# Optimization experiments

Measured on AMD Instinct MI355X. Metric: run time of the kernel, lower is better.

The kernel has to match this reference:

```python
import jax, jax.numpy as jnp
import numpy as np
from jax import lax

B, T = 2, 2048
HID = 2048
H, K, KC = 16, 128, 4
D = H * K  # projection dim
EPS = 1e-5
SCALE = K ** -0.5


def causal_conv_silu(x, w, b):
    # x: [B,T,D], depthwise causal conv, w: [D,KC], b: [D]
    xp = jnp.pad(jnp.swapaxes(x, 1, 2), ((0, 0), (0, 0), (KC - 1, 0)))  # [B,D,T+KC-1]
    y = lax.conv_general_dilated(xp, w[:, None, :], (1,), 'VALID', feature_group_count=D)
    return jax.nn.silu(jnp.swapaxes(y, 1, 2) + b)


def l2norm(x):
    return x * lax.rsqrt(jnp.sum(x * x, -1, keepdims=True) + 1e-6)


def kda_scan(q, k, v, g, beta):
    # gated delta-rule linear recurrence (KDA), per-key-dim log decay g
    # q,k,v,g: [B,T,H,K]; beta: [B,T,H]
    qT, kT, vT, gT, bT = (jnp.moveaxis(a, 1, 0) for a in (q, k, v, g, beta))
    S0 = jnp.zeros((q.shape[0], H, K, K), q.dtype)  # state [B,H,K,V]

    def step(S, inp):
        qt, kt, vt, gt, bt = inp
        S = S * jnp.exp(gt)[..., None]                                   # decay along K
        vd = (vt - jnp.einsum('bhkv,bhk->bhv', S, kt)) * bt[..., None]   # delta-rule error * beta
        S = S + kt[..., None] * vd[:, :, None, :]                        # rank-1 update
        return S, jnp.einsum('bhkv,bhk->bhv', S, qt)

    _, o = lax.scan(step, S0, (qT, kT, vT, gT, bT))
    return jnp.moveaxis(o, 0, 1)  # [B,T,H,K]


def _forward(x, Wq, Wk, Wv, conv_q_w, conv_q_b, conv_k_w, conv_k_b, conv_v_w, conv_v_b,
             Wfa, Wfb, A_log, dt_bias, Wb, Wga, Wgb, o_norm_w, Wo):
    b, t = x.shape[:2]
    q = causal_conv_silu(x @ Wq, conv_q_w, conv_q_b).reshape(b, t, H, K)
    k = causal_conv_silu(x @ Wk, conv_k_w, conv_k_b).reshape(b, t, H, K)
    v = causal_conv_silu(x @ Wv, conv_v_w, conv_v_b).reshape(b, t, H, K)
    # fine-grained decay gate: g = -exp(A_log[h]) * softplus(f_b(f_a(x)) + dt_bias)
    g = jax.nn.softplus((x @ Wfa) @ Wfb + dt_bias).reshape(b, t, H, K)
    g = -jnp.exp(A_log)[None, None, :, None] * g
    beta = jax.nn.sigmoid(x @ Wb)  # [B,T,H]
    q = l2norm(q) * SCALE
    k = l2norm(k)
    o = kda_scan(q, k, v, g, beta)  # [B,T,H,K]
    # gated head-wise RMSNorm
    gate = ((x @ Wga) @ Wgb).reshape(b, t, H, K)
    var = jnp.mean(o * o, -1, keepdims=True)
    o = o * lax.rsqrt(var + EPS) * o_norm_w * jax.nn.sigmoid(gate)
    return o.reshape(b, t, D) @ Wo


def setup_inputs() -> dict:
    key = jax.random.key(0)
    ks = jax.random.split(key, 16)
    s = 0.02
    f32 = jnp.float32
    return {
        'x': jax.random.normal(ks[0], (B, T, HID), f32),
        'Wq': jax.random.normal(ks[1], (HID, D), f32) * s,
        'Wk': jax.random.normal(ks[2], (HID, D), f32) * s,
        'Wv': jax.random.normal(ks[3], (HID, D), f32) * s,
        'conv_q_w': jax.random.normal(ks[4], (D, KC), f32) * 0.2,
        'conv_q_b': jnp.zeros((D,), f32),
        'conv_k_w': jax.random.normal(ks[5], (D, KC), f32) * 0.2,
        'conv_k_b': jnp.zeros((D,), f32),
        'conv_v_w': jax.random.normal(ks[6], (D, KC), f32) * 0.2,
        'conv_v_b': jnp.zeros((D,), f32),
        'Wfa': jax.random.normal(ks[7], (HID, K), f32) * s,
        'Wfb': jax.random.normal(ks[8], (K, D), f32) * s,
        'A_log': jnp.log(jax.random.uniform(ks[9], (H,), f32, 1.0, 16.0)),
        'dt_bias': jnp.zeros((D,), f32),
        'Wb': jax.random.normal(ks[10], (HID, H), f32) * s,
        'Wga': jax.random.normal(ks[11], (HID, K), f32) * s,
        'Wgb': jax.random.normal(ks[12], (K, D), f32) * s,
        'o_norm_w': jnp.ones((K,), f32),
        'Wo': jax.random.normal(ks[13], (D, HID), f32) * s,
    }


def reference(x, Wq, Wk, Wv, conv_q_w, conv_q_b, conv_k_w, conv_k_b, conv_v_w, conv_v_b,
              Wfa, Wfb, A_log, dt_bias, Wb, Wga, Wgb, o_norm_w, Wo):
    return _forward(x, Wq, Wk, Wv, conv_q_w, conv_q_b, conv_k_w, conv_k_b, conv_v_w, conv_v_b,
                    Wfa, Wfb, A_log, dt_bias, Wb, Wga, Wgb, o_norm_w, Wo)
```

## Files before the change

kernel.cpp:

```cpp
#include <hip/hip_runtime.h>
#include <cstddef>

#define Bsz 2
#define Tt  2048
#define HIDc 2048
#define Hh  16
#define Kc  128
#define Dc  2048
#define BT  (Bsz*Tt)
#define TS  8

typedef __attribute__((ext_vector_type(8))) __bf16 bf16x8;
typedef __attribute__((ext_vector_type(4))) __bf16 bf16x4;
typedef __attribute__((ext_vector_type(4))) float f32x4;

__device__ __forceinline__ float epilogue(float vacc, int c, int mode,
                                          const float* __restrict__ alog,
                                          const float* __restrict__ dtb) {
    if (mode == 1) {
        float z  = vacc + dtb[c];
        float sp = fmaxf(z, 0.f) + log1pf(expf(-fabsf(z)));
        return expf(-expf(alog[c >> 7]) * sp);
    } else if (mode == 2) {
        return 1.f / (1.f + expf(-vacc));
    }
    return vacc;
}

__global__ __launch_bounds__(256) void gemm_bf16_mfma(
    const __bf16* __restrict__ A, const __bf16* __restrict__ Bw,
    float* __restrict__ C, int M, int N, int K)
{
    __shared__ __bf16 As[128 * 64];
    __shared__ __bf16 Bs[128 * 64];
    const int tid = threadIdx.x;
    const int lane = tid & 63;
    const int wave = tid >> 6;
    const int wr = wave >> 1, wc = wave & 1;
    const int l15 = lane & 15, g = lane >> 4;
    const int row0 = blockIdx.y * 128, col0 = blockIdx.x * 128;

    f32x4 acc[4][4];
#pragma unroll
    for (int m = 0; m < 4; m++)
#pragma unroll
        for (int n = 0; n < 4; n++)
            acc[m][n] = (f32x4){0.f, 0.f, 0.f, 0.f};

    for (int k0 = 0; k0 < K; k0 += 64) {
        __syncthreads();
#pragma unroll
        for (int i = 0; i < 4; i++) {
            const int c = i * 256 + tid;
            const int row = c >> 3, kc = c & 7;
            const int scol = k0 + 8 * (kc ^ (row & 7));
            __builtin_amdgcn_global_load_lds(
                (const __attribute__((address_space(1))) void*)(A + (size_t)(row0 + row) * K + scol),
                (__attribute__((address_space(3))) void*)(As + (size_t)(i * 256 + (tid & ~63)) * 8),
                16, 0, 0);
        }
#pragma unroll
        for (int i = 0; i < 4; i++) {
            const int c = i * 256 + tid;
            const int row = c >> 3, kc = c & 7;
            const int scol = k0 + 8 * (kc ^ (row & 7));
            __builtin_amdgcn_global_load_lds(
                (const __attribute__((address_space(1))) void*)(Bw + (size_t)(col0 + row) * K + scol),
                (__attribute__((address_space(3))) void*)(Bs + (size_t)(i * 256 + (tid & ~63)) * 8),
                16, 0, 0);
        }
        __syncthreads();
#pragma unroll
        for (int ks = 0; ks < 2; ks++) {
            bf16x8 af[4], bfr[4];
#pragma unroll
            for (int m = 0; m < 4; m++) {
                const int row = wr * 64 + m * 16 + l15;
                const int kc = ks * 4 + g;
                af[m] = *(const bf16x8*)(As + row * 64 + 8 * (kc ^ (row & 7)));
            }
#pragma unroll
            for (int n = 0; n < 4; n++) {
                const int col = wc * 64 + n * 16 + l15;
                const int kc = ks * 4 + g;
                bfr[n] = *(const bf16x8*)(Bs + col * 64 + 8 * (kc ^ (col & 7)));
            }
#pragma unroll
            for (int m = 0; m < 4; m++)
#pragma unroll
                for (int n = 0; n < 4; n++)
                    acc[m][n] = __builtin_amdgcn_mfma_f32_16x16x32_bf16(
                        af[m], bfr[n], acc[m][n], 0, 0, 0);
        }
    }
#pragma unroll
    for (int m = 0; m < 4; m++) {
        const int rbase = row0 + wr * 64 + m * 16 + g * 4;
#pragma unroll
        for (int n = 0; n < 4; n++) {
            const int col = col0 + wc * 64 + n * 16 + l15;
#pragma unroll
            for (int r = 0; r < 4; r++)
                C[(size_t)(rbase + r) * N + col] = acc[m][n][r];
        }
    }
}

__global__ __launch_bounds__(256) void cvt_bf16(
    const float* __restrict__ in, __bf16* __restrict__ o)
{
    const int i = blockIdx.x * 256 + threadIdx.x;
    float4 v = *(const float4*)(in + (size_t)4 * i);
    bf16x4 r;
    r[0] = (__bf16)v.x; r[1] = (__bf16)v.y; r[2] = (__bf16)v.z; r[3] = (__bf16)v.w;
    *(bf16x4*)(o + (size_t)4 * i) = r;
}

__global__ __launch_bounds__(256) void transpose_to_bf16(
    const float* __restrict__ W, __bf16* __restrict__ WT, int Kd, int N)
{
    __shared__ float tile[32][33];
    const int n0 = blockIdx.x * 32, k0 = blockIdx.y * 32;
    const int tx = threadIdx.x & 31, ty = threadIdx.x >> 5;
#pragma unroll
    for (int i = 0; i < 4; i++)
        tile[ty + 8 * i][tx] = W[(size_t)(k0 + ty + 8 * i) * N + n0 + tx];
    __syncthreads();
#pragma unroll
    for (int i = 0; i < 4; i++)
        WT[(size_t)(n0 + ty + 8 * i) * Kd + k0 + tx] = (__bf16)tile[tx][ty + 8 * i];
}

__global__ __launch_bounds__(256) void gemm_f32(
    const float* __restrict__ A, const float* __restrict__ B, float* __restrict__ C,
    int M, int N, int Kd, int mode,
    const float* __restrict__ alog, const float* __restrict__ dtb)
{
    __shared__ float As[8][128];
    __shared__ float Bs[8][128];
    const int tid = threadIdx.x;
    const int tx = tid & 15, ty = tid >> 4;
    const int rbase = blockIdx.y * 128, cbase = blockIdx.x * 128;
    const int z = blockIdx.z, Znum = gridDim.z;
    const int kchunk = Kd / Znum;
    const int kbeg = z * kchunk, kend = kbeg + kchunk;

    float acc[8][8];
#pragma unroll
    for (int i = 0; i < 8; i++)
#pragma unroll
        for (int j = 0; j < 8; j++) acc[i][j] = 0.f;

    const int arow = tid >> 1, ak = (tid & 1) << 2;
    const int bk = tid >> 5, bn = (tid & 31) << 2;

    for (int k0 = kbeg; k0 < kend; k0 += 8) {
        float4 av = *(const float4*)(A + (size_t)(rbase + arow) * Kd + (k0 + ak));
        float4 bv = make_float4(0.f, 0.f, 0.f, 0.f);
        if (cbase + bn < N)
            bv = *(const float4*)(B + (size_t)(k0 + bk) * N + (cbase + bn));
        __syncthreads();
        As[ak + 0][arow] = av.x;
        As[ak + 1][arow] = av.y;
        As[ak + 2][arow] = av.z;
        As[ak + 3][arow] = av.w;
        *(float4*)(&Bs[bk][bn]) = bv;
        __syncthreads();
#pragma unroll
        for (int kk = 0; kk < 8; ++kk) {
            float a[8], bb[8];
            *(float4*)(&a[0]) = *(const float4*)(&As[kk][ty << 2]);
            *(float4*)(&a[4]) = *(const float4*)(&As[kk][64 + (ty << 2)]);
            *(float4*)(&bb[0]) = *(const float4*)(&Bs[kk][tx << 2]);
            *(float4*)(&bb[4]) = *(const float4*)(&Bs[kk][64 + (tx << 2)]);
#pragma unroll
            for (int i = 0; i < 8; i++)
#pragma unroll
                for (int j = 0; j < 8; j++)
                    acc[i][j] = fmaf(a[i], bb[j], acc[i][j]);
        }
    }

    if (Znum > 1) {
        float* P = C + (size_t)z * M * N;
#pragma unroll
        for (int ih = 0; ih < 2; ih++)
#pragma unroll
            for (int i = 0; i < 4; i++) {
                int r = rbase + ih * 64 + (ty << 2) + i;
#pragma unroll
                for (int jh = 0; jh < 2; jh++) {
                    int c0 = cbase + jh * 64 + (tx << 2);
                    if (c0 < N) {
                        float4 vv;
                        vv.x = acc[ih * 4 + i][jh * 4 + 0];
                        vv.y = acc[ih * 4 + i][jh * 4 + 1];
                        vv.z = acc[ih * 4 + i][jh * 4 + 2];
                        vv.w = acc[ih * 4 + i][jh * 4 + 3];
                        *(float4*)(P + (size_t)r * N + c0) = vv;
                    }
                }
            }
    } else {
#pragma unroll
        for (int ih = 0; ih < 2; ih++)
#pragma unroll
            for (int i = 0; i < 4; i++) {
                int r = rbase + ih * 64 + (ty << 2) + i;
#pragma unroll
                for (int jh = 0; jh < 2; jh++) {
                    int c0 = cbase + jh * 64 + (tx << 2);
                    if (c0 < N) {
                        float4 vv;
                        vv.x = epilogue(acc[ih * 4 + i][jh * 4 + 0], c0 + 0, mode, alog, dtb);
                        vv.y = epilogue(acc[ih * 4 + i][jh * 4 + 1], c0 + 1, mode, alog, dtb);
                        vv.z = epilogue(acc[ih * 4 + i][jh * 4 + 2], c0 + 2, mode, alog, dtb);
                        vv.w = epilogue(acc[ih * 4 + i][jh * 4 + 3], c0 + 3, mode, alog, dtb);
                        *(float4*)(C + (size_t)r * N + c0) = vv;
                    }
                }
            }
    }
}

__global__ __launch_bounds__(256) void reduce_k(
    const float* __restrict__ part, float* __restrict__ out,
    int MN, int Z, int N, int mode,
    const float* __restrict__ alog, const float* __restrict__ dtb)
{
    int i = blockIdx.x * 256 + threadIdx.x;
    if (i < MN) {
        float s = 0.f;
        for (int zz = 0; zz < Z; zz++) s += part[(size_t)zz * MN + i];
        out[i] = epilogue(s, i % N, mode, alog, dtb);
    }
}

__global__ __launch_bounds__(128) void conv_silu_norm(
    const float* __restrict__ pre, const float* __restrict__ cw,
    const float* __restrict__ cb, float* __restrict__ out, int mode)
{
    const int bid = blockIdx.x;
    const int h = bid & (Hh - 1);
    const int bt = bid >> 4;
    const int t = bt & (Tt - 1);
    const int lane = threadIdx.x;
    const int col = h * Kc + lane;
    const float w0 = cw[col * 4 + 0], w1 = cw[col * 4 + 1];
    const float w2 = cw[col * 4 + 2], w3 = cw[col * 4 + 3];
    const float* bp = pre + (size_t)bt * Dc + col;
    float acc = cb[col] + w3 * bp[0];
    if (t >= 1) acc += w2 * bp[-Dc];
    if (t >= 2) acc += w1 * bp[-2 * Dc];
    if (t >= 3) acc += w0 * bp[-3 * Dc];
    float val = acc / (1.f + expf(-acc));
    if (mode) {
        float ss = val * val;
#pragma unroll
        for (int m = 1; m < 64; m <<= 1) ss += __shfl_xor(ss, m);
        __shared__ float p2[2];
        if ((lane & 63) == 0) p2[lane >> 6] = ss;
        __syncthreads();
        float tot = p2[0] + p2[1];
        float r = rsqrtf(tot + 1e-6f);
        val *= r;
        if (mode == 2) val *= 0.08838834764831845f;
    }
    out[(size_t)bt * Dc + col] = val;
}

template <int CTRL>
__device__ __forceinline__ float dpp_add(float v) {
    return __int_as_float(__builtin_amdgcn_update_dpp(
        0, __float_as_int(v), CTRL, 0xf, 0xf, true));
}

__device__ __forceinline__ void reduce3_row(float& a, float& b, float& c) {
    a += dpp_add<0xB1>(a);
    b += dpp_add<0xB1>(b);
    c += dpp_add<0xB1>(c);
    a += dpp_add<0x4E>(a);
    b += dpp_add<0x4E>(b);
    c += dpp_add<0x4E>(c);
    a += dpp_add<0x124>(a);
    b += dpp_add<0x124>(b);
    c += dpp_add<0x124>(c);
    a += dpp_add<0x128>(a);
    b += dpp_add<0x128>(b);
    c += dpp_add<0x128>(c);
}

__device__ __forceinline__ float kda_step(
    const float4 cq[2], const float4 ck[2], const float4 cd[2],
    float cv, float cbt, float S[8])
{
    float kv0 = 0.f, kv1 = 0.f, qs0 = 0.f, qs1 = 0.f, qk0 = 0.f, qk1 = 0.f;
#pragma unroll
    for (int i = 0; i < 2; i++) {
        S[4 * i + 0] *= cd[i].x;
        S[4 * i + 1] *= cd[i].y;
        S[4 * i + 2] *= cd[i].z;
        S[4 * i + 3] *= cd[i].w;
        kv0 = fmaf(ck[i].x, S[4 * i + 0], kv0);
        kv1 = fmaf(ck[i].y, S[4 * i + 1], kv1);
        kv0 = fmaf(ck[i].z, S[4 * i + 2], kv0);
        kv1 = fmaf(ck[i].w, S[4 * i + 3], kv1);
        qs0 = fmaf(cq[i].x, S[4 * i + 0], qs0);
        qs1 = fmaf(cq[i].y, S[4 * i + 1], qs1);
        qs0 = fmaf(cq[i].z, S[4 * i + 2], qs0);
        qs1 = fmaf(cq[i].w, S[4 * i + 3], qs1);
        qk0 = fmaf(ck[i].x, cq[i].x, qk0);
        qk1 = fmaf(ck[i].y, cq[i].y, qk1);
        qk0 = fmaf(ck[i].z, cq[i].z, qk0);
        qk1 = fmaf(ck[i].w, cq[i].w, qk1);
    }
    float kv = kv0 + kv1, qs = qs0 + qs1, qk = qk0 + qk1;
    reduce3_row(kv, qs, qk);
    float vd = (cv - kv) * cbt;
    float ov = fmaf(qk, vd, qs);
#pragma unroll
    for (int i = 0; i < 2; i++) {
        S[4 * i + 0] = fmaf(ck[i].x, vd, S[4 * i + 0]);
        S[4 * i + 1] = fmaf(ck[i].y, vd, S[4 * i + 1]);
        S[4 * i + 2] = fmaf(ck[i].z, vd, S[4 * i + 2]);
        S[4 * i + 3] = fmaf(ck[i].w, vd, S[4 * i + 3]);
    }
    return ov;
}

__device__ __forceinline__ void kda_tile(
    const float (&sm)[3][TS * 128], const float (&vm)[TS * 4],
    const float (&bm)[TS], float S[8], int kq, int vloc,
    float* __restrict__ op, int lane)
{
    float4 cq[2], ck[2], cd[2];
    float cv, cb;
#pragma unroll
    for (int i = 0; i < 2; i++) {
        cq[i] = *(const float4*)&sm[0][(kq * 2 + i) * 4];
        ck[i] = *(const float4*)&sm[1][(kq * 2 + i) * 4];
        cd[i] = *(const float4*)&sm[2][(kq * 2 + i) * 4];
    }
    cv = vm[vloc];
    cb = bm[0];
#pragma unroll
    for (int t = 0; t < TS; ++t) {
        float4 nq[2], nk[2], nd[2];
        float nv = 0.f, nb = 0.f;
        if (t + 1 < TS) {
#pragma unroll
            for (int i = 0; i < 2; i++) {
                nq[i] = *(const float4*)&sm[0][(t + 1) * 128 + (kq * 2 + i) * 4];
                nk[i] = *(const float4*)&sm[1][(t + 1) * 128 + (kq * 2 + i) * 4];
                nd[i] = *(const float4*)&sm[2][(t + 1) * 128 + (kq * 2 + i) * 4];
            }
            nv = vm[(t + 1) * 4 + vloc];
            nb = bm[t + 1];
        }
        const float ov = kda_step(cq, ck, cd, cv, cb, S);
        if ((lane & 15) == 0)
            op[(size_t)t * Dc + vloc] = ov;
        if (t + 1 < TS) {
#pragma unroll
            for (int i = 0; i < 2; i++) { cq[i] = nq[i]; ck[i] = nk[i]; cd[i] = nd[i]; }
            cv = nv; cb = nb;
        }
    }
}

__global__ __launch_bounds__(64, 2) void kda_scan_kernel(
    const float* __restrict__ q, const float* __restrict__ k,
    const float* __restrict__ v, const float* __restrict__ dec,
    const float* __restrict__ beta, float* __restrict__ o)
{
    __shared__ float sA[3][TS * 128];
    __shared__ float sB[3][TS * 128];
    __shared__ float vA[TS * 4], vB[TS * 4];
    __shared__ float bA[TS], bB[TS];

    const int bid = blockIdx.x;
    const int r8 = bid & 7;
    const int s = bid >> 3;
    const int bh = r8 + 8 * (s >> 5);
    const int vc = s & 31;
    const int h = bh & (Hh - 1);
    const int b = bh >> 4;
    const int lane = threadIdx.x;
    const int vloc = lane >> 4;
    const int kq = lane & 15;
    const size_t base = ((size_t)b * Tt) * Dc + h * Kc;
    const size_t bbase = ((size_t)b * Tt) * Hh + h;

    float S[8];
#pragma unroll
    for (int i = 0; i < 8; i++) S[i] = 0.f;

    const int s_t = lane >> 5;
    const int s_w = lane & 31;

#define STAGE(TILE, SM, VM, BM)                                                 \
    {                                                                           \
        _Pragma("unroll")                                                       \
        for (int r = 0; r < 4; r++) {                                           \
            const size_t rb = base + (size_t)((TILE) * TS + 2 * r + s_t) * Dc   \
                              + s_w * 4;                                        \
            __builtin_amdgcn_global_load_lds(                                   \
                (const __attribute__((address_space(1))) void*)(q + rb),        \
                (__attribute__((address_space(3))) void*)(&SM[0][r * 256]),     \
                16, 0, 0);                                                      \
            __builtin_amdgcn_global_load_lds(                                   \
                (const __attribute__((address_space(1))) void*)(k + rb),        \
                (__attribute__((address_space(3))) void*)(&SM[1][r * 256]),     \
                16, 0, 0);                                                      \
            __builtin_amdgcn_global_load_lds(                                   \
                (const __attribute__((address_space(1))) void*)(dec + rb),      \
                (__attribute__((address_space(3))) void*)(&SM[2][r * 256]),     \
                16, 0, 0);                                                      \
        }                                                                       \
        if (lane < 32)                                                          \
            __builtin_amdgcn_global_load_lds(                                   \
                (const __attribute__((address_space(1))) void*)(v + base        \
                    + (size_t)((TILE) * TS + (lane >> 2)) * Dc + vc * 4         \
                    + (lane & 3)),                                              \
                (__attribute__((address_space(3))) void*)(&VM[0]), 4, 0, 0);    \
        if (lane < TS)                                                          \
            __builtin_amdgcn_global_load_lds(                                   \
                (const __attribute__((address_space(1))) void*)(beta + bbase    \
                    + (size_t)((TILE) * TS + lane) * Hh),                       \
                (__attribute__((address_space(3))) void*)(&BM[0]), 4, 0, 0);    \
    }

    STAGE(0, sA, vA, bA);
    asm volatile("s_waitcnt vmcnt(0)" ::: "memory");
    __builtin_amdgcn_sched_barrier(0);

    const int NT = Tt / TS;
    for (int tile = 0; tile < NT; tile += 2) {
        if (tile + 1 < NT) STAGE(tile + 1, sB, vB, bB);
        kda_tile(sA, vA, bA, S, kq, vloc,
                 o + base + (size_t)tile * TS * Dc + vc * 4, lane);
        asm volatile("s_waitcnt vmcnt(0)" ::: "memory");
        __builtin_amdgcn_sched_barrier(0);
        if (tile + 2 < NT) STAGE(tile + 2, sA, vA, bA);
        kda_tile(sB, vB, bB, S, kq, vloc,
                 o + base + (size_t)(tile + 1) * TS * Dc + vc * 4, lane);
        asm volatile("s_waitcnt vmcnt(0)" ::: "memory");
        __builtin_amdgcn_sched_barrier(0);
    }
#undef STAGE
}

__global__ __launch_bounds__(128) void post_norm(
    const float* __restrict__ o, const float* __restrict__ gate,
    const float* __restrict__ onw, float* __restrict__ og)
{
    const int bid = blockIdx.x;
    const int h = bid & (Hh - 1);
    const int bt = bid >> 4;
    const int lane = threadIdx.x;
    size_t idx = (size_t)bt * Dc + h * Kc + lane;
    float ov = o[idx];
    float ss = ov * ov;
#pragma unroll
    for (int m = 1; m < 64; m <<= 1) ss += __shfl_xor(ss, m);
    __shared__ float p2[2];
    if ((lane & 63) == 0) p2[lane >> 6] = ss;
    __syncthreads();
    float var = (p2[0] + p2[1]) * (1.f / 128.f);
    float r = rsqrtf(var + 1e-5f);
    float gt = gate[idx];
    og[idx] = ov * r * onw[lane] * (1.f / (1.f + expf(-gt)));
}

extern "C" void kernel_launch(void* const* d_in, const int* in_sizes, int n_in,
                              void* d_out, int out_size, void* d_ws, size_t ws_size,
                              hipStream_t stream) {
    const float* x        = (const float*)d_in[0];
    const float* Wq       = (const float*)d_in[1];
    const float* Wk       = (const float*)d_in[2];
    const float* Wv       = (const float*)d_in[3];
    const float* conv_q_w = (const float*)d_in[4];
    const float* conv_q_b = (const float*)d_in[5];
    const float* conv_k_w = (const float*)d_in[6];
    const float* conv_k_b = (const float*)d_in[7];
    const float* conv_v_w = (const float*)d_in[8];
    const float* conv_v_b = (const float*)d_in[9];
    const float* Wfa      = (const float*)d_in[10];
    const float* Wfb      = (const float*)d_in[11];
    const float* A_log    = (const float*)d_in[12];
    const float* dt_bias  = (const float*)d_in[13];
    const float* Wb       = (const float*)d_in[14];
    const float* Wga      = (const float*)d_in[15];
    const float* Wgb      = (const float*)d_in[16];
    const float* o_norm_w = (const float*)d_in[17];
    const float* Wo       = (const float*)d_in[18];
    float* out = (float*)d_out;

    float* ws = (float*)d_ws;
    const size_t SZ = (size_t)BT * Dc;
    float* bufA = ws + 0 * SZ;
    float* bufB = ws + 1 * SZ;
    float* bufC = ws + 2 * SZ;
    float* bufG = ws + 3 * SZ;
    float* bufQ = ws + 4 * SZ;
    float* bufI = ws + 5 * SZ;
    float* fa   = ws + 6 * SZ;
    float* ga   = fa + (size_t)BT * Kc;
    float* beta = ga + (size_t)BT * Kc;
    __bf16* xb = (__bf16*)(beta + (size_t)BT * Hh);
    __bf16* wT = xb + SZ;

    dim3 blk(256);
    cvt_bf16<<<dim3(SZ / 1024), blk, 0, stream>>>(x, xb);
    dim3 tgrid(Dc / 32, HIDc / 32);
    dim3 gbig(Dc / 128, BT / 128);
    transpose_to_bf16<<<tgrid, blk, 0, stream>>>(Wq, wT, HIDc, Dc);
    gemm_bf16_mfma<<<gbig, blk, 0, stream>>>(xb, wT, bufA, BT, Dc, HIDc);
    transpose_to_bf16<<<tgrid, blk, 0, stream>>>(Wk, wT, HIDc, Dc);
    gemm_bf16_mfma<<<gbig, blk, 0, stream>>>(xb, wT, bufB, BT, Dc, HIDc);
    transpose_to_bf16<<<tgrid, blk, 0, stream>>>(Wv, wT, HIDc, Dc);
    gemm_bf16_mfma<<<gbig, blk, 0, stream>>>(xb, wT, bufC, BT, Dc, HIDc);
    dim3 gskin(1, 32, 8);
    gemm_f32<<<gskin, blk, 0, stream>>>(x, Wfa, bufI, BT, Kc, HIDc, 0, nullptr, nullptr);
    reduce_k<<<dim3((BT * Kc + 255) / 256), blk, 0, stream>>>(bufI, fa, BT * Kc, 8, Kc, 0, nullptr, nullptr);
    gemm_f32<<<gskin, blk, 0, stream>>>(x, Wga, bufI, BT, Kc, HIDc, 0, nullptr, nullptr);
    reduce_k<<<dim3((BT * Kc + 255) / 256), blk, 0, stream>>>(bufI, ga, BT * Kc, 8, Kc, 0, nullptr, nullptr);
    gemm_f32<<<gskin, blk, 0, stream>>>(x, Wb, bufI, BT, Hh, HIDc, 0, nullptr, nullptr);
    reduce_k<<<dim3((BT * Hh + 255) / 256), blk, 0, stream>>>(bufI, beta, BT * Hh, 8, Hh, 2, nullptr, nullptr);
    dim3 gmid(Dc / 128, BT / 128);
    gemm_f32<<<gmid, blk, 0, stream>>>(fa, Wfb, bufG, BT, Dc, Kc, 1, A_log, dt_bias);
    gemm_f32<<<gmid, blk, 0, stream>>>(ga, Wgb, bufI, BT, Dc, Kc, 0, nullptr, nullptr);
    dim3 cblk(128);
    dim3 cgrid(BT * Hh);
    conv_silu_norm<<<cgrid, cblk, 0, stream>>>(bufA, conv_q_w, conv_q_b, bufQ, 2);
    conv_silu_norm<<<cgrid, cblk, 0, stream>>>(bufB, conv_k_w, conv_k_b, bufA, 1);
    conv_silu_norm<<<cgrid, cblk, 0, stream>>>(bufC, conv_v_w, conv_v_b, bufB, 0);
    kda_scan_kernel<<<dim3(1024), dim3(64), 0, stream>>>(bufQ, bufA, bufB, bufG, beta, bufC);
    post_norm<<<cgrid, cblk, 0, stream>>>(bufC, bufI, o_norm_w, bufG);
    transpose_to_bf16<<<tgrid, blk, 0, stream>>>(Wo, wT, Dc, HIDc);
    cvt_bf16<<<dim3(SZ / 1024), blk, 0, stream>>>(bufG, xb);
    dim3 gout(HIDc / 128, BT / 128);
    gemm_bf16_mfma<<<gout, blk, 0, stream>>>(xb, wT, out, BT, HIDc, Dc);
}
```

Before: 1.134 ms.

## Triple-buffer KDA scan staging, fuse skinny projections, emit bf16 from post-norm

The scan kernel moves from a double-buffered to a triple-buffered LDS pipeline that prefetches two tiles ahead and uses partial vmcnt waits instead of full drains, to hide global load latency in the sequential recurrence. The three skinny projections (Wfa, Wga, Wb) are packed into one concatenated weight and done in a single split-K GEMM plus one reduction, with the sigmoid for beta applied only to the last columns. Post-norm now writes bf16 directly, which drops the separate conversion pass before the output GEMM. The trade-offs are more LDS per scan block, which may reduce occupancy, hand-tuned vmcnt counts that must match the exact number of outstanding loads, and an extra weight-packing kernel on every call.

```diff
diff --git a/kernel.cpp b/kernel.cpp
--- a/kernel.cpp
+++ b/kernel.cpp
@@ -9,6 +9,7 @@
 #define Dc  2048
 #define BT  (Bsz*Tt)
 #define TS  8
+#define FGBs 272
 
 typedef __attribute__((ext_vector_type(8))) __bf16 bf16x8;
 typedef __attribute__((ext_vector_type(4))) __bf16 bf16x4;
@@ -23,6 +24,8 @@
         return expf(-expf(alog[c >> 7]) * sp);
     } else if (mode == 2) {
         return 1.f / (1.f + expf(-vacc));
+    } else if (mode == 3) {
+        return (c >= 256) ? 1.f / (1.f + expf(-vacc)) : vacc;
     }
     return vacc;
 }
@@ -131,9 +134,23 @@
         WT[(size_t)(n0 + ty + 8 * i) * Kd + k0 + tx] = (__bf16)tile[tx][ty + 8 * i];
 }
 
+__global__ __launch_bounds__(256) void pack_fgb(
+    const float* __restrict__ Wfa, const float* __restrict__ Wga,
+    const float* __restrict__ Wb, float* __restrict__ Bcat)
+{
+    const int i = blockIdx.x * 256 + threadIdx.x;
+    if (i >= HIDc * FGBs) return;
+    const int k = i / FGBs, c = i % FGBs;
+    float v;
+    if (c < 128)      v = Wfa[k * 128 + c];
+    else if (c < 256) v = Wga[k * 128 + (c - 128)];
+    else              v = Wb[k * 16 + (c - 256)];
+    Bcat[i] = v;
+}
+
 __global__ __launch_bounds__(256) void gemm_f32(
     const float* __restrict__ A, const float* __restrict__ B, float* __restrict__ C,
-    int M, int N, int Kd, int mode,
+    int M, int N, int Kd, int lda, int mode,
     const float* __restrict__ alog, const float* __restrict__ dtb)
 {
     __shared__ float As[8][128];
@@ -155,7 +172,7 @@
     const int bk = tid >> 5, bn = (tid & 31) << 2;
 
     for (int k0 = kbeg; k0 < kend; k0 += 8) {
-        float4 av = *(const float4*)(A + (size_t)(rbase + arow) * Kd + (k0 + ak));
+        float4 av = *(const float4*)(A + (size_t)(rbase + arow) * lda + (k0 + ak));
         float4 bv = make_float4(0.f, 0.f, 0.f, 0.f);
         if (cbase + bn < N)
             bv = *(const float4*)(B + (size_t)(k0 + bk) * N + (cbase + bn));
@@ -329,8 +346,8 @@
 }
 
 __device__ __forceinline__ void kda_tile(
-    const float (&sm)[3][TS * 128], const float (&vm)[TS * 4],
-    const float (&bm)[TS], float S[8], int kq, int vloc,
+    const float (*sm)[TS * 128], const float* vm,
+    const float* bm, float S[8], int kq, int vloc,
     float* __restrict__ op, int lane)
 {
     float4 cq[2], ck[2], cd[2];
@@ -371,12 +388,13 @@
 __global__ __launch_bounds__(64, 2) void kda_scan_kernel(
     const float* __restrict__ q, const float* __restrict__ k,
     const float* __restrict__ v, const float* __restrict__ dec,
-    const float* __restrict__ beta, float* __restrict__ o)
+    const float* __restrict__ fgb, float* __restrict__ o)
 {
     __shared__ float sA[3][TS * 128];
     __shared__ float sB[3][TS * 128];
-    __shared__ float vA[TS * 4], vB[TS * 4];
-    __shared__ float bA[TS], bB[TS];
+    __shared__ float sC[3][TS * 128];
+    __shared__ float vA[TS * 4], vB[TS * 4], vC[TS * 4];
+    __shared__ float bA[TS], bB[TS], bC[TS];
 
     const int bid = blockIdx.x;
     const int r8 = bid & 7;
@@ -389,7 +407,7 @@
     const int vloc = lane >> 4;
     const int kq = lane & 15;
     const size_t base = ((size_t)b * Tt) * Dc + h * Kc;
-    const size_t bbase = ((size_t)b * Tt) * Hh + h;
+    const size_t bbase = ((size_t)b * Tt) * FGBs + 256 + h;
 
     float S[8];
 #pragma unroll
@@ -425,26 +443,36 @@
                 (__attribute__((address_space(3))) void*)(&VM[0]), 4, 0, 0);    \
         if (lane < TS)                                                          \
             __builtin_amdgcn_global_load_lds(                                   \
-                (const __attribute__((address_space(1))) void*)(beta + bbase    \
-                    + (size_t)((TILE) * TS + lane) * Hh),                       \
+                (const __attribute__((address_space(1))) void*)(fgb + bbase     \
+                    + (size_t)((TILE) * TS + lane) * FGBs),                     \
                 (__attribute__((address_space(3))) void*)(&BM[0]), 4, 0, 0);    \
     }
 
     STAGE(0, sA, vA, bA);
-    asm volatile("s_waitcnt vmcnt(0)" ::: "memory");
+    STAGE(1, sB, vB, bB);
+    asm volatile("s_waitcnt vmcnt(14)" ::: "memory");
     __builtin_amdgcn_sched_barrier(0);
 
     const int NT = Tt / TS;
-    for (int tile = 0; tile < NT; tile += 2) {
-        if (tile + 1 < NT) STAGE(tile + 1, sB, vB, bB);
-        kda_tile(sA, vA, bA, S, kq, vloc,
+    for (int tile = 0; tile < NT; ++tile) {
+        if (tile + 2 < NT) {
+            const int r2 = (tile + 2) % 3;
+            float (*sT)[TS * 128] = (r2 == 0) ? sA : (r2 == 1) ? sB : sC;
+            float* vT = (r2 == 0) ? vA : (r2 == 1) ? vB : vC;
+            float* bT = (r2 == 0) ? bA : (r2 == 1) ? bB : bC;
+            STAGE(tile + 2, sT, vT, bT);
+            __builtin_amdgcn_sched_barrier(0);
+        }
+        const int rr = tile % 3;
+        const float (*sm)[TS * 128] = (rr == 0) ? sA : (rr == 1) ? sB : sC;
+        const float* vm = (rr == 0) ? vA : (rr == 1) ? vB : vC;
+        const float* bm = (rr == 0) ? bA : (rr == 1) ? bB : bC;
+        kda_tile(sm, vm, bm, S, kq, vloc,
                  o + base + (size_t)tile * TS * Dc + vc * 4, lane);
-        asm volatile("s_waitcnt vmcnt(0)" ::: "memory");
-        __builtin_amdgcn_sched_barrier(0);
-        if (tile + 2 < NT) STAGE(tile + 2, sA, vA, bA);
-        kda_tile(sB, vB, bB, S, kq, vloc,
-                 o + base + (size_t)(tile + 1) * TS * Dc + vc * 4, lane);
-        asm volatile("s_waitcnt vmcnt(0)" ::: "memory");
+        if (tile + 2 < NT)
+            asm volatile("s_waitcnt vmcnt(22)" ::: "memory");
+        else
+            asm volatile("s_waitcnt vmcnt(8)" ::: "memory");
         __builtin_amdgcn_sched_barrier(0);
     }
 #undef STAGE
@@ -452,7 +480,7 @@
 
 __global__ __launch_bounds__(128) void post_norm(
     const float* __restrict__ o, const float* __restrict__ gate,
-    const float* __restrict__ onw, float* __restrict__ og)
+    const float* __restrict__ onw, __bf16* __restrict__ og)
 {
     const int bid = blockIdx.x;
     const int h = bid & (Hh - 1);
@@ -469,7 +497,7 @@
     float var = (p2[0] + p2[1]) * (1.f / 128.f);
     float r = rsqrtf(var + 1e-5f);
     float gt = gate[idx];
-    og[idx] = ov * r * onw[lane] * (1.f / (1.f + expf(-gt)));
+    og[idx] = (__bf16)(ov * r * onw[lane] * (1.f / (1.f + expf(-gt))));
 }
 
 extern "C" void kernel_launch(void* const* d_in, const int* in_sizes, int n_in,
@@ -504,14 +532,14 @@
     float* bufG = ws + 3 * SZ;
     float* bufQ = ws + 4 * SZ;
     float* bufI = ws + 5 * SZ;
-    float* fa   = ws + 6 * SZ;
-    float* ga   = fa + (size_t)BT * Kc;
-    float* beta = ga + (size_t)BT * Kc;
-    __bf16* xb = (__bf16*)(beta + (size_t)BT * Hh);
+    float* fgb  = ws + 6 * SZ;
+    __bf16* xb = (__bf16*)(fgb + (size_t)BT * FGBs);
     __bf16* wT = xb + SZ;
+    float* Bcat = (float*)(wT + (size_t)HIDc * Dc);
 
     dim3 blk(256);
     cvt_bf16<<<dim3(SZ / 1024), blk, 0, stream>>>(x, xb);
+    pack_fgb<<<dim3((HIDc * FGBs + 255) / 256), blk, 0, stream>>>(Wfa, Wga, Wb, Bcat);
     dim3 tgrid(Dc / 32, HIDc / 32);
     dim3 gbig(Dc / 128, BT / 128);
     transpose_to_bf16<<<tgrid, blk, 0, stream>>>(Wq, wT, HIDc, Dc);
@@ -520,25 +548,20 @@
     gemm_bf16_mfma<<<gbig, blk, 0, stream>>>(xb, wT, bufB, BT, Dc, HIDc);
     transpose_to_bf16<<<tgrid, blk, 0, stream>>>(Wv, wT, HIDc, Dc);
     gemm_bf16_mfma<<<gbig, blk, 0, stream>>>(xb, wT, bufC, BT, Dc, HIDc);
-    dim3 gskin(1, 32, 8);
-    gemm_f32<<<gskin, blk, 0, stream>>>(x, Wfa, bufI, BT, Kc, HIDc, 0, nullptr, nullptr);
-    reduce_k<<<dim3((BT * Kc + 255) / 256), blk, 0, stream>>>(bufI, fa, BT * Kc, 8, Kc, 0, nullptr, nullptr);
-    gemm_f32<<<gskin, blk, 0, stream>>>(x, Wga, bufI, BT, Kc, HIDc, 0, nullptr, nullptr);
-    reduce_k<<<dim3((BT * Kc + 255) / 256), blk, 0, stream>>>(bufI, ga, BT * Kc, 8, Kc, 0, nullptr, nullptr);
-    gemm_f32<<<gskin, blk, 0, stream>>>(x, Wb, bufI, BT, Hh, HIDc, 0, nullptr, nullptr);
-    reduce_k<<<dim3((BT * Hh + 255) / 256), blk, 0, stream>>>(bufI, beta, BT * Hh, 8, Hh, 2, nullptr, nullptr);
+    dim3 gskin(3, 32, 8);
+    gemm_f32<<<gskin, blk, 0, stream>>>(x, Bcat, bufQ, BT, FGBs, HIDc, HIDc, 0, nullptr, nullptr);
+    reduce_k<<<dim3((BT * FGBs + 255) / 256), blk, 0, stream>>>(bufQ, fgb, BT * FGBs, 8, FGBs, 3, nullptr, nullptr);
     dim3 gmid(Dc / 128, BT / 128);
-    gemm_f32<<<gmid, blk, 0, stream>>>(fa, Wfb, bufG, BT, Dc, Kc, 1, A_log, dt_bias);
-    gemm_f32<<<gmid, blk, 0, stream>>>(ga, Wgb, bufI, BT, Dc, Kc, 0, nullptr, nullptr);
+    gemm_f32<<<gmid, blk, 0, stream>>>(fgb, Wfb, bufG, BT, Dc, Kc, FGBs, 1, A_log, dt_bias);
+    gemm_f32<<<gmid, blk, 0, stream>>>(fgb + 128, Wgb, bufI, BT, Dc, Kc, FGBs, 0, nullptr, nullptr);
     dim3 cblk(128);
     dim3 cgrid(BT * Hh);
     conv_silu_norm<<<cgrid, cblk, 0, stream>>>(bufA, conv_q_w, conv_q_b, bufQ, 2);
     conv_silu_norm<<<cgrid, cblk, 0, stream>>>(bufB, conv_k_w, conv_k_b, bufA, 1);
     conv_silu_norm<<<cgrid, cblk, 0, stream>>>(bufC, conv_v_w, conv_v_b, bufB, 0);
-    kda_scan_kernel<<<dim3(1024), dim3(64), 0, stream>>>(bufQ, bufA, bufB, bufG, beta, bufC);
-    post_norm<<<cgrid, cblk, 0, stream>>>(bufC, bufI, o_norm_w, bufG);
+    kda_scan_kernel<<<dim3(1024), dim3(64), 0, stream>>>(bufQ, bufA, bufB, bufG, fgb, bufC);
+    post_norm<<<cgrid, cblk, 0, stream>>>(bufC, bufI, o_norm_w, xb);
     transpose_to_bf16<<<tgrid, blk, 0, stream>>>(Wo, wT, Dc, HIDc);
-    cvt_bf16<<<dim3(SZ / 1024), blk, 0, stream>>>(bufG, xb);
     dim3 gout(HIDc / 128, BT / 128);
     gemm_bf16_mfma<<<gout, blk, 0, stream>>>(xb, wT, out, BT, HIDc, Dc);
 }
```

After: 984.2 us. 1.15x faster.
